# Kernel tuning notes

Hardware: AMD Instinct MI355X
Metric: run time of the kernel (lower is better)

The kernel has to match this reference:

```python
import jax, jax.numpy as jnp
import numpy as np

B, L, D, C, NL = 32, 512, 768, 97, 2  # batch, seq_len, hidden, class_nums, gat_layers


def setup_inputs() -> dict:
    key = jax.random.key(0)
    ks = jax.random.split(key, 16)

    def n(k, shape, scale=0.02):
        return jax.random.normal(k, shape, dtype=jnp.float32) * scale

    return dict(
        x=n(ks[0], (B, L, D), 1.0),                 # encoder output
        pos1=jnp.ones((B, L), jnp.float32),          # entity-1 position mask
        pos2=jnp.ones((B, L), jnp.float32),          # entity-2 position mask
        mask=jnp.ones((B, L), jnp.int32),            # attention mask (1 = keep)
        emb=n(ks[1], (C, D), 1.0),                   # relation label embedding table
        rel_w=n(ks[2], (D, D)), rel_b=jnp.zeros((D,), jnp.float32),
        # per-layer, per-RA (axis1: 0=ra1, 1=ra2) parameters
        qw=n(ks[3], (NL, 2, D, D)), qb=jnp.zeros((NL, 2, D), jnp.float32),
        kw=n(ks[4], (NL, 2, D, D)), kb=jnp.zeros((NL, 2, D), jnp.float32),
        vw=n(ks[5], (NL, 2, D, D)), vb=jnp.zeros((NL, 2, D), jnp.float32),
        sw=n(ks[6], (NL, 2, 2 * D)), sb=jnp.zeros((NL, 2), jnp.float32),   # score: Linear(2d,1)
        gw=n(ks[7], (NL, 2, 2 * D)), gb=jnp.zeros((NL, 2), jnp.float32),   # gate:  Linear(2d,1)
        fc1_w=n(ks[8], (3 * D, D)), fc1_b=jnp.zeros((D,), jnp.float32),
        fc2_w=n(ks[9], (D,)), fc2_b=jnp.zeros((), jnp.float32),
    )


def _relation_attention(p, x, qw, qb, kw, kb, vw, vb, sw, sb, gw, gb, mask):
    # p: (b, c, d) queries; x: (b, l, d) keys/values
    d = p.shape[-1]
    q = jnp.einsum('bcd,de->bce', p, qw) + qb          # (b, c, d)
    k = jnp.einsum('bld,de->ble', x, kw) + kb          # (b, l, d)
    # score = Linear(concat([q_i, k_j])) is separable: q@sw[:d] + k@sw[d:] + sb
    score = (q @ sw[:d])[:, :, None] + (k @ sw[d:])[:, None, :] + sb  # (b, c, l)
    if mask is not None:
        score = jnp.where(mask[:, None, :] == 0, jnp.float32(-1e9), score)
    attn = jax.nn.softmax(score, axis=2)
    v = jnp.einsum('bld,de->ble', x, vw) + vb          # (b, l, d)
    out = jnp.einsum('bcl,bld->bcd', attn, v) + p      # (b, c, d)
    # gate = sigmoid(Linear(concat([out, p]))), also separable
    g = jax.nn.sigmoid(out @ gw[:d] + p @ gw[d:] + gb)[..., None]
    return g * out + (1.0 - g) * p


def reference(x, pos1, pos2, mask, emb, rel_w, rel_b,
              qw, qb, kw, kb, vw, vb, sw, sb, gw, gb,
              fc1_w, fc1_b, fc2_w, fc2_b):
    b, d = x.shape[0], x.shape[-1]
    # p = relation(embedding(arange(C))) broadcast over batch
    p = emb @ rel_w + rel_b                            # (C, d)
    p = jnp.broadcast_to(p[None], (b,) + p.shape)      # (b, C, d)

    for li in range(qw.shape[0]):
        x = _relation_attention(x, p, qw[li, 0], qb[li, 0], kw[li, 0], kb[li, 0],
                                vw[li, 0], vb[li, 0], sw[li, 0], sb[li, 0],
                                gw[li, 0], gb[li, 0], None) + x
        p = _relation_attention(p, x, qw[li, 1], qb[li, 1], kw[li, 1], kb[li, 1],
                                vw[li, 1], vb[li, 1], sw[li, 1], sb[li, 1],
                                gw[li, 1], gb[li, 1], mask) + p

    def pool_avg(pos):
        return jnp.sum(x * pos[:, :, None], axis=1) / jnp.sum(pos, axis=1)[:, None]

    e1 = pool_avg(pos1)                                # (b, d)
    e2 = pool_avg(pos2)                                # (b, d)
    cshape = p.shape                                   # (b, C, d)
    pc = jnp.concatenate([p,
                          jnp.broadcast_to(e1[:, None, :], cshape),
                          jnp.broadcast_to(e2[:, None, :], cshape)], axis=2)  # (b, C, 3d)
    h = jnp.tanh(pc @ fc1_w + fc1_b)                   # (b, C, d)
    logits = jax.nn.sigmoid(h @ fc2_w + fc2_b)         # (b, C)
    pred = jnp.argmax(logits, axis=1)                  # (b,)
    return logits, pred
```

## Files before the change

### kernel.cpp

```cpp
#include <hip/hip_runtime.h>
#include <math.h>

#define NBLK 512
#define NTHR 256
static const int Bb = 32, Ls = 512, Dd = 768, Cc = 97;

struct KArgs {
    const float *x0, *pos1, *pos2;
    const int* mask;
    const float *emb, *rel_w, *rel_b, *kw, *vw, *vb, *sw, *gw, *gb;
    const float *fc1w, *fc1b, *fc2w, *fc2b;
    float* out;
    float *p0b, *pp, *sc, *avx1, *avx2, *av1, *av2, *aw1, *aw2, *S0, *S1, *xp1, *xp2, *geb;
    float *kvecs, *pdots, *g1buf, *xd, *gx1, *gx2, *awb;
    float* zbase;
    int zcount;
};

__device__ __forceinline__ float sigm(float x) { return 1.f / (1.f + expf(-x)); }

__device__ __forceinline__ float wred(float v) {
#pragma unroll
    for (int o = 32; o > 0; o >>= 1) v += __shfl_down(v, o, 64);
    return v;
}

__device__ __forceinline__ float blk_sum4(float v, float* shr) {
    v = wred(v);
    int t = threadIdx.x;
    if ((t & 63) == 0) shr[t >> 6] = v;
    __syncthreads();
    float r = shr[0] + shr[1] + shr[2] + shr[3];
    __syncthreads();
    return r;
}

__device__ void sgemm_dev(const float* __restrict__ A, const float* __restrict__ W,
                          const float* __restrict__ bias, float* __restrict__ C,
                          int M, int N, int K, int KC, int bx, int by, int bz,
                          float* As, float* Ws) {
    int tid = threadIdx.x;
    int tx = tid & 15, ty = tid >> 4;
    int bn = bx * 64, bm = by * 64;
    int kb = bz * KC;
    int arow = tid >> 2, akq = (tid & 3) << 2;
    int wrow = tid >> 4, wcol = (tid & 15) << 2;
    int gar = bm + arow;
    bool aval = gar < M;
    const float* Ap = A + (size_t)gar * K + kb + akq;
    const float* Wp = W + (size_t)(kb + wrow) * N + bn + wcol;
    float acc[4][4] = {{0.f}};
    float4 a4 = make_float4(0.f, 0.f, 0.f, 0.f);
    if (aval) a4 = *(const float4*)Ap;
    float4 w4 = *(const float4*)Wp;
    for (int k0 = 0; k0 < KC; k0 += 16) {
        __syncthreads();
        As[(akq + 0) * 64 + arow] = a4.x; As[(akq + 1) * 64 + arow] = a4.y;
        As[(akq + 2) * 64 + arow] = a4.z; As[(akq + 3) * 64 + arow] = a4.w;
        *(float4*)&Ws[wrow * 64 + wcol] = w4;
        __syncthreads();
        if (k0 + 16 < KC) {
            if (aval) a4 = *(const float4*)(Ap + k0 + 16);
            w4 = *(const float4*)(Wp + (size_t)(k0 + 16) * N);
        }
#pragma unroll
        for (int kk = 0; kk < 16; ++kk) {
            float4 a = *(const float4*)&As[kk * 64 + (ty << 2)];
            float4 b = *(const float4*)&Ws[kk * 64 + (tx << 2)];
            acc[0][0]+=a.x*b.x; acc[0][1]+=a.x*b.y; acc[0][2]+=a.x*b.z; acc[0][3]+=a.x*b.w;
            acc[1][0]+=a.y*b.x; acc[1][1]+=a.y*b.y; acc[1][2]+=a.y*b.z; acc[1][3]+=a.y*b.w;
            acc[2][0]+=a.z*b.x; acc[2][1]+=a.z*b.y; acc[2][2]+=a.z*b.z; acc[2][3]+=a.z*b.w;
            acc[3][0]+=a.w*b.x; acc[3][1]+=a.w*b.y; acc[3][2]+=a.w*b.z; acc[3][3]+=a.w*b.w;
        }
    }
    int gc = bn + (tx << 2);
    float4 bz4 = make_float4(0.f, 0.f, 0.f, 0.f);
    if (bz == 0 && bias) bz4 = *(const float4*)(bias + gc);
#pragma unroll
    for (int i = 0; i < 4; ++i) {
        int gr = bm + (ty << 2) + i;
        if (gr < M) {
            float* cp = C + (size_t)gr * N + gc;
            atomicAdd(cp + 0, acc[i][0] + bz4.x); atomicAdd(cp + 1, acc[i][1] + bz4.y);
            atomicAdd(cp + 2, acc[i][2] + bz4.z); atomicAdd(cp + 3, acc[i][3] + bz4.w);
        }
    }
}

__device__ void attn_gemv(const KArgs& a, int phase, int jlin,
                          float* xs, float* lw, float* shr) {
    int t = threadIdx.x;
    int jseg = jlin % 3, b = (jlin / 3) % 32, seg = jlin / 96;
    float v = -3.0e38f, g1 = 0.f;
    if (t < Cc) {
        if (phase == 0) v = a.pdots[t];
        else {
            g1 = sigm(a.pdots[194 + t] + a.sc[128 + b] + a.gb[1]);
            v = 2.f * a.pdots[97 + t] + g1 * a.sc[160 + b];
        }
    }
    if (phase == 1 && jseg == 0 && seg == 0 && t < Cc) a.g1buf[(size_t)b * Cc + t] = g1;
    float m = v;
#pragma unroll
    for (int o = 32; o > 0; o >>= 1) m = fmaxf(m, __shfl_down(m, o, 64));
    if ((t & 63) == 0) shr[t >> 6] = m;
    __syncthreads();
    m = fmaxf(fmaxf(shr[0], shr[1]), fmaxf(shr[2], shr[3]));
    __syncthreads();
    float e = (t < Cc) ? expf(v - m) : 0.f;
    float s = blk_sum4(e, shr);
    float wc = e / s;
    if (t < Cc) lw[t] = wc;
    float cg1 = blk_sum4(wc * g1, shr);
    float alpha = (phase == 0) ? 1.f : 2.f;
    if (t < 192) {
        int d = seg * 192 + t;
        const float* pc = a.p0b + d;
        float acc2 = 0.f;
        for (int c = 0; c < Cc; ++c) acc2 += lw[c] * pc[(size_t)c * Dd];
        float val = alpha * acc2;
        if (phase == 1) val += cg1 * a.av1[(size_t)b * Dd + d];
        xs[t] = val;
    }
    __syncthreads();
    const float* W = a.vw + (size_t)(phase == 0 ? 0 : 2) * Dd * Dd;
    const float* bias = a.vb + (phase == 0 ? 0 : 2) * Dd;
    float* outp = (phase == 0) ? a.avx1 : a.avx2;
    int j = jseg * 256 + t;
    float acc = (seg == 0) ? bias[j] : 0.f;
    const float* wp = W + (size_t)(seg * 192) * Dd + j;
#pragma unroll 4
    for (int dd = 0; dd < 192; ++dd) acc += xs[dd] * wp[(size_t)dd * Dd];
    atomicAdd(&outp[(size_t)b * Dd + j], acc);
    const float* da[4]; const float* db[4]; int nd; float* dout;
    if (phase == 0) {
        da[0]=a.gw;          db[0]=nullptr;
        da[1]=a.kvecs+Dd;    db[1]=nullptr;
        da[2]=a.gw+3072;     db[2]=a.gw+3840;
        da[3]=a.kvecs+3*Dd;  db[3]=nullptr;
        nd = 4; dout = a.sc;
    } else {
        da[0]=a.gw+3072;     db[0]=nullptr;
        da[1]=a.kvecs+3*Dd;  db[1]=nullptr;
        nd = 2; dout = a.sc + 224;
    }
    for (int vv = 0; vv < nd; ++vv) {
        float wv = da[vv][j] + (db[vv] ? db[vv][j] : 0.f);
        float p = blk_sum4(acc * wv, shr);
        if (t == 0) atomicAdd(&dout[vv * 32 + b], p);
    }
}

__device__ void mm_dev(const KArgs& a, int jlin, const float* S, float gamma,
                       const float* avA, const float* coefA, float multA,
                       const float* avB, const float* coefB, float multB,
                       const float* W, const float* bias, float* outp,
                       int ndots, const float* d0a, const float* d0b,
                       const float* d1a, const float* d2a, const float* d2b,
                       float* dout, float* xs, float* shr) {
    int t = threadIdx.x;
    int jseg = jlin % 3, b = (jlin / 3) % 32, seg = jlin / 96;
    if (t < 192) {
        int d = seg * 192 + t;
        float v = gamma * S[(size_t)b * Dd + d];
        if (avA) v += multA * coefA[b] * avA[(size_t)b * Dd + d];
        if (avB) v += multB * coefB[b] * avB[(size_t)b * Dd + d];
        xs[t] = v;
    }
    __syncthreads();
    int j = jseg * 256 + t;
    float acc = (seg == 0 && bias) ? bias[j] : 0.f;
    const float* wp = W + (size_t)(seg * 192) * Dd + j;
#pragma unroll 4
    for (int dd = 0; dd < 192; ++dd) acc += xs[dd] * wp[(size_t)dd * Dd];
    atomicAdd(&outp[(size_t)b * Dd + j], acc);
    if (ndots > 0) {
        float wv = d0a[j] + (d0b ? d0b[j] : 0.f);
        float p = blk_sum4(acc * wv, shr);
        if (t == 0) atomicAdd(&dout[b], p);
    }
    if (ndots > 1) {
        float p = blk_sum4(acc * d1a[j], shr);
        if (t == 0) atomicAdd(&dout[32 + b], p);
    }
    if (ndots > 2) {
        float wv = d2a[j] + (d2b ? d2b[j] : 0.f);
        float p = blk_sum4(acc * wv, shr);
        if (t == 0) atomicAdd(&dout[64 + b], p);
    }
    __syncthreads();
}

__device__ void ge_dev(const KArgs& a, int jlin, float* xs, float* xs2) {
    __syncthreads();
    int t = threadIdx.x;
    int jseg = jlin % 3, b = (jlin / 3) % 32, seg = jlin / 96;
    if (t < 192) {
        int d = seg * 192 + t;
        float a1 = a.avx1[(size_t)b * Dd + d], a2 = a.avx2[(size_t)b * Dd + d];
        xs[t]  = (4.f * a.xp1[(size_t)b * Dd + d] + 2.f * a.sc[448 + b] * a1 + a.sc[480 + b] * a2) * a.sc[576 + b];
        xs2[t] = (4.f * a.xp2[(size_t)b * Dd + d] + 2.f * a.sc[512 + b] * a1 + a.sc[544 + b] * a2) * a.sc[608 + b];
    }
    __syncthreads();
    int j = jseg * 256 + t;
    float a1 = 0.f, a2 = 0.f;
    const float* w1 = a.fc1w + (size_t)(Dd + seg * 192) * Dd + j;
    const float* w2 = a.fc1w + (size_t)(2 * Dd + seg * 192) * Dd + j;
#pragma unroll 4
    for (int dd = 0; dd < 192; ++dd) {
        a1 += xs[dd] * w1[(size_t)dd * Dd];
        a2 += xs2[dd] * w2[(size_t)dd * Dd];
    }
    float res = a1 + a2 + (seg == 0 ? a.fc1b[j] : 0.f);
    atomicAdd(&a.geb[(size_t)b * Dd + j], res);
}

__device__ void softgate_dev(const KArgs& a, int phase, int b, float* shr) {
    int t = threadIdx.x;
    float ks[2], ga[2] = {0.f, 0.f}, gb2[2] = {0.f, 0.f};
#pragma unroll
    for (int i = 0; i < 2; ++i) {
        int l = t + (i << 8);
        size_t r = (size_t)b * Ls + l;
        float4 x = *(const float4*)(a.xd + r * 4);
        if (phase == 0) {
            float g = sigm(x.x + a.sc[b] + a.gb[0]);
            a.gx1[r] = g;
            ga[i] = g;
            ks[i] = 2.f * x.y + g * a.sc[32 + b];
        } else {
            float gp = a.gx1[r];
            float g = sigm(2.f * x.z + gp * a.sc[64 + b] + a.sc[224 + b] + a.gb[2]);
            a.gx2[r] = g;
            ga[i] = gp; gb2[i] = g;
            ks[i] = 4.f * x.w + 2.f * gp * a.sc[96 + b] + g * a.sc[256 + b];
        }
        if (a.mask[r] == 0) ks[i] = -1e9f;
    }
    float mx = fmaxf(ks[0], ks[1]);
#pragma unroll
    for (int o = 32; o > 0; o >>= 1) mx = fmaxf(mx, __shfl_down(mx, o, 64));
    if ((t & 63) == 0) shr[t >> 6] = mx;
    __syncthreads();
    mx = fmaxf(fmaxf(shr[0], shr[1]), fmaxf(shr[2], shr[3]));
    __syncthreads();
    float e0 = expf(ks[0] - mx), e1 = expf(ks[1] - mx);
    float s = blk_sum4(e0 + e1, shr);
    float inv = 1.f / s;
    float w0 = e0 * inv, w1 = e1 * inv;
    a.awb[(size_t)b * Ls + t] = w0;
    a.awb[(size_t)b * Ls + t + 256] = w1;
    float ca = blk_sum4(w0 * ga[0] + w1 * ga[1], shr);
    if (phase == 0) {
        if (t == 0) a.sc[320 + b] = ca;
    } else {
        if (t == 0) a.sc[352 + b] = ca;
        float cb = blk_sum4(w0 * gb2[0] + w1 * gb2[1], shr);
        if (t == 0) a.sc[384 + b] = cb;
        float q1a = a.pos1[(size_t)b * Ls + t], q1b = a.pos1[(size_t)b * Ls + t + 256];
        float q2a = a.pos2[(size_t)b * Ls + t], q2b = a.pos2[(size_t)b * Ls + t + 256];
        float s1 = blk_sum4(q1a + q1b, shr);
        float s2 = blk_sum4(q2a + q2b, shr);
        float c11 = blk_sum4(q1a * ga[0] + q1b * ga[1], shr);
        float c12 = blk_sum4(q1a * gb2[0] + q1b * gb2[1], shr);
        float c21 = blk_sum4(q2a * ga[0] + q2b * ga[1], shr);
        float c22 = blk_sum4(q2a * gb2[0] + q2b * gb2[1], shr);
        if (t == 0) {
            a.sc[448 + b] = c11; a.sc[480 + b] = c12;
            a.sc[512 + b] = c21; a.sc[544 + b] = c22;
            a.sc[576 + b] = 1.f / s1; a.sc[608 + b] = 1.f / s2;
        }
    }
}

__device__ void passX_dev(const KArgs& a, int blk, float* S, bool dopos) {
    int t = threadIdx.x;
    int b = blk >> 4, seg = blk & 15, l0 = seg * 32;
    const float* xb = a.x0 + ((size_t)b * Ls + l0) * Dd;
    const float* wb = a.awb + (size_t)b * Ls + l0;
    float s0 = 0.f, s1 = 0.f, s2 = 0.f;
    float p10 = 0.f, p11 = 0.f, p12 = 0.f, p20 = 0.f, p21 = 0.f, p22 = 0.f;
    for (int l = 0; l < 32; ++l) {
        float wv = wb[l];
        float x_0 = xb[(size_t)l * Dd + t];
        float x_1 = xb[(size_t)l * Dd + t + 256];
        float x_2 = xb[(size_t)l * Dd + t + 512];
        s0 += wv * x_0; s1 += wv * x_1; s2 += wv * x_2;
        if (dopos) {
            float q1 = a.pos1[(size_t)b * Ls + l0 + l], q2 = a.pos2[(size_t)b * Ls + l0 + l];
            p10 += q1 * x_0; p11 += q1 * x_1; p12 += q1 * x_2;
            p20 += q2 * x_0; p21 += q2 * x_1; p22 += q2 * x_2;
        }
    }
    atomicAdd(&S[(size_t)b * Dd + t], s0);
    atomicAdd(&S[(size_t)b * Dd + t + 256], s1);
    atomicAdd(&S[(size_t)b * Dd + t + 512], s2);
    if (dopos) {
        atomicAdd(&a.xp1[(size_t)b * Dd + t], p10);
        atomicAdd(&a.xp1[(size_t)b * Dd + t + 256], p11);
        atomicAdd(&a.xp1[(size_t)b * Dd + t + 512], p12);
        atomicAdd(&a.xp2[(size_t)b * Dd + t], p20);
        atomicAdd(&a.xp2[(size_t)b * Dd + t + 256], p21);
        atomicAdd(&a.xp2[(size_t)b * Dd + t + 512], p22);
    }
}

__global__ void k_zero_kvec(KArgs a) {
    int blk = blockIdx.x, t = threadIdx.x;
    int wv_ = t >> 6, lane = t & 63;
    for (size_t i = (size_t)blk * NTHR + t; i < (size_t)a.zcount; i += (size_t)NBLK * NTHR)
        a.zbase[i] = 0.f;
    int g = blk * 4 + wv_;
    for (int rep = 0; rep < 2; ++rep) {
        int dot = g + rep * 2048;
        if (dot < 3072) {
            int idx = dot / Dd, d = dot - idx * Dd;
            const float* row = a.kw + ((size_t)idx * Dd + d) * Dd;
            const float* swk = a.sw + (size_t)idx * 2 * Dd + Dd;
            float sA = 0.f;
            for (int j = lane; j < Dd; j += 64) sA += row[j] * swk[j];
            sA = wred(sA);
            if (lane == 0) a.kvecs[dot] = sA;
        }
    }
}

__global__ void k_gemm1(KArgs a) {
    __shared__ float As[1024], Ws[1024];
    int blk = blockIdx.x;
    sgemm_dev(a.emb, a.rel_w, a.rel_b, a.p0b, Cc, Dd, Dd, 96,
              blk % 12, (blk / 12) % 2, blk / 24, As, Ws);
}

__global__ void k_prep2(KArgs a) {
    __shared__ float As[1024], Ws[1024];
    int blk = blockIdx.x, t = threadIdx.x;
    int wv_ = t >> 6, lane = t & 63;
    if (blk < 96) {
        sgemm_dev(a.p0b, a.fc1w, nullptr, a.pp, Cc, Dd, Dd, 192,
                  blk % 12, (blk / 12) % 2, blk / 24, As, Ws);
    } else if (blk < 128) {
        int g2 = (blk - 96) * 4 + wv_;
        for (int k = 0; k < 4; ++k) {
            int j = g2 + k * 128;
            if (k == 3) { if (g2 >= 4) break; j = 384 + g2; }
            if (j >= 388) continue;
            int vv = j / Cc, r = j - vv * Cc;
            const float* va; const float* vb2 = nullptr;
            if (vv == 0) va = a.kvecs;
            else if (vv == 1) va = a.kvecs + 2 * Dd;
            else if (vv == 2) { va = a.gw + 1536; vb2 = a.gw + 2304; }
            else { va = a.gw + 4608; vb2 = a.gw + 5376; }
            const float* row = a.p0b + (size_t)r * Dd;
            float sA = 0.f;
            for (int jj = lane; jj < Dd; jj += 64)
                sA += row[jj] * (va[jj] + (vb2 ? vb2[jj] : 0.f));
            sA = wred(sA);
            if (lane == 0) a.pdots[j] = sA;
        }
    } else {
        float gs0[12], k1r[12], gs2[12], k3r[12];
#pragma unroll
        for (int k = 0; k < 12; ++k) {
            int d = lane + k * 64;
            gs0[k] = a.gw[d] + a.gw[768 + d];
            k1r[k] = a.kvecs[768 + d];
            gs2[k] = a.gw[3072 + d] + a.gw[3840 + d];
            k3r[k] = a.kvecs[2304 + d];
        }
        int gwv = (blk - 128) * 4 + wv_;
        for (int r = gwv; r < Bb * Ls; r += 1536) {
            const float* xr = a.x0 + (size_t)r * Dd;
            float s0 = 0.f, s1 = 0.f, s2 = 0.f, s3 = 0.f;
#pragma unroll
            for (int k = 0; k < 12; ++k) {
                float xv = xr[lane + k * 64];
                s0 += xv * gs0[k]; s1 += xv * k1r[k];
                s2 += xv * gs2[k]; s3 += xv * k3r[k];
            }
            s0 = wred(s0); s1 = wred(s1); s2 = wred(s2); s3 = wred(s3);
            if (lane == 0) {
                float4 o4 = make_float4(s0, s1, s2, s3);
                *(float4*)(a.xd + (size_t)r * 4) = o4;
            }
        }
    }
}

__global__ void k_attn(KArgs a, int phase) {
    __shared__ float xs[192], lw[128], shr[16];
    attn_gemv(a, phase, blockIdx.x, xs, lw, shr);
}

__global__ void k_softgate(KArgs a, int phase) {
    __shared__ float shr[16];
    softgate_dev(a, phase, blockIdx.x, shr);
}

__global__ void k_passX(KArgs a, int which) {
    passX_dev(a, blockIdx.x, which == 0 ? a.S0 : a.S1, which == 0);
}

__global__ void k_mm0(KArgs a) {
    __shared__ float xs[192], shr[16];
    mm_dev(a, blockIdx.x, a.S0, 2.f, a.avx1, a.sc + 320, 1.f, nullptr, nullptr, 0.f,
           a.vw + (size_t)1 * Dd * Dd, a.vb + Dd, a.av1,
           3, a.gw + 1536, nullptr, a.kvecs + 2 * Dd, a.gw + 4608, a.gw + 5376,
           a.sc + 128, xs, shr);
}

__global__ void k_mm1ge(KArgs a) {
    __shared__ float xs[192], xs2[192], shr[16];
    int blk = blockIdx.x;
    if (blk < 384)
        mm_dev(a, blk, a.S1, 4.f, a.avx1, a.sc + 352, 2.f, a.avx2, a.sc + 384, 1.f,
               a.vw + (size_t)3 * Dd * Dd, a.vb + 3 * Dd, a.av2,
               1, a.gw + 4608, nullptr, nullptr, nullptr, nullptr,
               a.sc + 288, xs, shr);
    if (blk >= 128) ge_dev(a, blk - 128, xs, xs2);
}

__global__ void k_aw(KArgs a) {
    __shared__ float xs[192], shr[16];
    int blk = blockIdx.x;
    if (blk < 384)
        mm_dev(a, blk, a.av1, 1.f, nullptr, nullptr, 0.f, nullptr, nullptr, 0.f,
               a.fc1w, nullptr, a.aw1, 0, nullptr, nullptr, nullptr, nullptr, nullptr,
               nullptr, xs, shr);
    else
        mm_dev(a, blk - 384, a.av2, 1.f, nullptr, nullptr, 0.f, nullptr, nullptr, 0.f,
               a.fc1w, nullptr, a.aw2, 0, nullptr, nullptr, nullptr, nullptr, nullptr,
               nullptr, xs, shr);
}

__global__ void k_logits(KArgs a) {
    __shared__ float shr[16];
    int blk = blockIdx.x, t = threadIdx.x;
    for (int r = blk; r < Bb * Cc; r += NBLK) {
        int b = r / Cc, c = r - b * Cc;
        float g1 = a.g1buf[r];
        float g2 = sigm(2.f * a.pdots[291 + c] + g1 * a.sc[192 + b] + a.sc[288 + b] + a.gb[3]);
        float ssum = 0.f;
#pragma unroll
        for (int sseg = 0; sseg < 3; ++sseg) {
            int d = t + sseg * 256;
            float h = tanhf(4.f * a.pp[(size_t)c * Dd + d]
                          + 2.f * g1 * a.aw1[(size_t)b * Dd + d]
                          + g2 * a.aw2[(size_t)b * Dd + d]
                          + a.geb[(size_t)b * Dd + d]);
            ssum += h * a.fc2w[d];
        }
        float tt = blk_sum4(ssum, shr);
        if (t == 0) a.out[r] = sigm(tt + a.fc2b[0]);
    }
}

__global__ void k_argmax(KArgs a) {
    int t = threadIdx.x;
    if (t < Bb) {
        const float* row = a.out + (size_t)t * Cc;
        float best = row[0];
        int bi = 0;
        for (int c = 1; c < Cc; ++c) {
            float v = row[c];
            if (v > best) { best = v; bi = c; }
        }
        a.out[Bb * Cc + t] = (float)bi;
    }
}

extern "C" void kernel_launch(void* const* d_in, const int* in_sizes, int n_in,
                              void* d_out, int out_size, void* d_ws, size_t ws_size,
                              hipStream_t stream) {
    KArgs ka;
    ka.x0    = (const float*)d_in[0];
    ka.pos1  = (const float*)d_in[1];
    ka.pos2  = (const float*)d_in[2];
    ka.mask  = (const int*)d_in[3];
    ka.emb   = (const float*)d_in[4];
    ka.rel_w = (const float*)d_in[5];
    ka.rel_b = (const float*)d_in[6];
    ka.kw    = (const float*)d_in[9];
    ka.vw    = (const float*)d_in[11];
    ka.vb    = (const float*)d_in[12];
    ka.sw    = (const float*)d_in[13];
    ka.gw    = (const float*)d_in[15];
    ka.gb    = (const float*)d_in[16];
    ka.fc1w  = (const float*)d_in[17];
    ka.fc1b  = (const float*)d_in[18];
    ka.fc2w  = (const float*)d_in[19];
    ka.fc2b  = (const float*)d_in[20];
    ka.out   = (float*)d_out;

    float* ws = (float*)d_ws;
    size_t off = 0;
    const size_t PD = (size_t)Cc * Dd;
    const size_t BD = (size_t)Bb * Dd;
    ka.p0b  = ws + off; off += PD;
    ka.pp   = ws + off; off += PD;
    ka.sc   = ws + off; off += 640;
    ka.avx1 = ws + off; off += BD;
    ka.avx2 = ws + off; off += BD;
    ka.av1  = ws + off; off += BD;
    ka.av2  = ws + off; off += BD;
    ka.aw1  = ws + off; off += BD;
    ka.aw2  = ws + off; off += BD;
    ka.S0   = ws + off; off += BD;
    ka.S1   = ws + off; off += BD;
    ka.xp1  = ws + off; off += BD;
    ka.xp2  = ws + off; off += BD;
    ka.geb  = ws + off; off += BD;
    ka.zbase = ws;
    ka.zcount = (int)off;
    ka.kvecs = ws + off; off += (size_t)4 * Dd;
    ka.pdots = ws + off; off += 388;
    ka.g1buf = ws + off; off += (size_t)Bb * Cc;
    ka.xd    = ws + off; off += (size_t)Bb * Ls * 4;
    ka.gx1   = ws + off; off += (size_t)Bb * Ls;
    ka.gx2   = ws + off; off += (size_t)Bb * Ls;
    ka.awb   = ws + off; off += (size_t)Bb * Ls;

    k_zero_kvec<<<NBLK, NTHR, 0, stream>>>(ka);
    k_gemm1<<<192, NTHR, 0, stream>>>(ka);
    k_prep2<<<NBLK, NTHR, 0, stream>>>(ka);
    k_attn<<<384, NTHR, 0, stream>>>(ka, 0);
    k_softgate<<<32, NTHR, 0, stream>>>(ka, 0);
    k_passX<<<NBLK, NTHR, 0, stream>>>(ka, 0);
    k_mm0<<<384, NTHR, 0, stream>>>(ka);
    k_attn<<<384, NTHR, 0, stream>>>(ka, 1);
    k_softgate<<<32, NTHR, 0, stream>>>(ka, 1);
    k_passX<<<NBLK, NTHR, 0, stream>>>(ka, 1);
    k_mm1ge<<<NBLK, NTHR, 0, stream>>>(ka);
    k_aw<<<768, NTHR, 0, stream>>>(ka);
    k_logits<<<NBLK, NTHR, 0, stream>>>(ka);
    k_argmax<<<1, 64, 0, stream>>>(ka);
}
```

Measured before the change: 383.9 us.

## Split GEMV K-range finer, vectorize passX/prep2, fuse aw dual and regroup kernels

The K segment of each GEMV shrinks from 192 to 96, so the attention, mm and ge kernels launch twice as many blocks, which adds parallelism at the cost of more atomic adds. passX and prep2 now use float4 loads. The two aw GEMVs are merged into one kernel that loads each fc1 weight once for both outputs. passX1 is launched together with ge, and mm1 becomes its own kernel, with launch bounds added throughout.

```diff
diff --git a/kernel.cpp b/kernel.cpp
--- a/kernel.cpp
+++ b/kernel.cpp
@@ -90,7 +90,7 @@
 __device__ void attn_gemv(const KArgs& a, int phase, int jlin,
                           float* xs, float* lw, float* shr) {
     int t = threadIdx.x;
-    int jseg = jlin % 3, b = (jlin / 3) % 32, seg = jlin / 96;
+    int jt = jlin % 3, b = (jlin / 3) % 32, kseg = jlin / 96;
     float v = -3.0e38f, g1 = 0.f;
     if (t < Cc) {
         if (phase == 0) v = a.pdots[t];
@@ -99,7 +99,7 @@
             v = 2.f * a.pdots[97 + t] + g1 * a.sc[160 + b];
         }
     }
-    if (phase == 1 && jseg == 0 && seg == 0 && t < Cc) a.g1buf[(size_t)b * Cc + t] = g1;
+    if (phase == 1 && jt == 0 && kseg == 0 && t < Cc) a.g1buf[(size_t)b * Cc + t] = g1;
     float m = v;
 #pragma unroll
     for (int o = 32; o > 0; o >>= 1) m = fmaxf(m, __shfl_down(m, o, 64));
@@ -113,10 +113,11 @@
     if (t < Cc) lw[t] = wc;
     float cg1 = blk_sum4(wc * g1, shr);
     float alpha = (phase == 0) ? 1.f : 2.f;
-    if (t < 192) {
-        int d = seg * 192 + t;
+    if (t < 96) {
+        int d = kseg * 96 + t;
         const float* pc = a.p0b + d;
         float acc2 = 0.f;
+#pragma unroll 4
         for (int c = 0; c < Cc; ++c) acc2 += lw[c] * pc[(size_t)c * Dd];
         float val = alpha * acc2;
         if (phase == 1) val += cg1 * a.av1[(size_t)b * Dd + d];
@@ -126,11 +127,11 @@
     const float* W = a.vw + (size_t)(phase == 0 ? 0 : 2) * Dd * Dd;
     const float* bias = a.vb + (phase == 0 ? 0 : 2) * Dd;
     float* outp = (phase == 0) ? a.avx1 : a.avx2;
-    int j = jseg * 256 + t;
-    float acc = (seg == 0) ? bias[j] : 0.f;
-    const float* wp = W + (size_t)(seg * 192) * Dd + j;
-#pragma unroll 4
-    for (int dd = 0; dd < 192; ++dd) acc += xs[dd] * wp[(size_t)dd * Dd];
+    int j = jt * 256 + t;
+    float acc = (kseg == 0) ? bias[j] : 0.f;
+    const float* wp = W + (size_t)(kseg * 96) * Dd + j;
+#pragma unroll 8
+    for (int dd = 0; dd < 96; ++dd) acc += xs[dd] * wp[(size_t)dd * Dd];
     atomicAdd(&outp[(size_t)b * Dd + j], acc);
     const float* da[4]; const float* db[4]; int nd; float* dout;
     if (phase == 0) {
@@ -159,20 +160,20 @@
                        const float* d1a, const float* d2a, const float* d2b,
                        float* dout, float* xs, float* shr) {
     int t = threadIdx.x;
-    int jseg = jlin % 3, b = (jlin / 3) % 32, seg = jlin / 96;
-    if (t < 192) {
-        int d = seg * 192 + t;
+    int jt = jlin % 3, b = (jlin / 3) % 32, kseg = jlin / 96;
+    if (t < 96) {
+        int d = kseg * 96 + t;
         float v = gamma * S[(size_t)b * Dd + d];
         if (avA) v += multA * coefA[b] * avA[(size_t)b * Dd + d];
         if (avB) v += multB * coefB[b] * avB[(size_t)b * Dd + d];
         xs[t] = v;
     }
     __syncthreads();
-    int j = jseg * 256 + t;
-    float acc = (seg == 0 && bias) ? bias[j] : 0.f;
-    const float* wp = W + (size_t)(seg * 192) * Dd + j;
-#pragma unroll 4
-    for (int dd = 0; dd < 192; ++dd) acc += xs[dd] * wp[(size_t)dd * Dd];
+    int j = jt * 256 + t;
+    float acc = (kseg == 0 && bias) ? bias[j] : 0.f;
+    const float* wp = W + (size_t)(kseg * 96) * Dd + j;
+#pragma unroll 8
+    for (int dd = 0; dd < 96; ++dd) acc += xs[dd] * wp[(size_t)dd * Dd];
     atomicAdd(&outp[(size_t)b * Dd + j], acc);
     if (ndots > 0) {
         float wv = d0a[j] + (d0b ? d0b[j] : 0.f);
@@ -188,31 +189,51 @@
         float p = blk_sum4(acc * wv, shr);
         if (t == 0) atomicAdd(&dout[64 + b], p);
     }
-    __syncthreads();
 }
 
 __device__ void ge_dev(const KArgs& a, int jlin, float* xs, float* xs2) {
-    __syncthreads();
-    int t = threadIdx.x;
-    int jseg = jlin % 3, b = (jlin / 3) % 32, seg = jlin / 96;
-    if (t < 192) {
-        int d = seg * 192 + t;
+    int t = threadIdx.x;
+    int jt = jlin % 3, b = (jlin / 3) % 32, kseg = jlin / 96;
+    if (t < 96) {
+        int d = kseg * 96 + t;
         float a1 = a.avx1[(size_t)b * Dd + d], a2 = a.avx2[(size_t)b * Dd + d];
         xs[t]  = (4.f * a.xp1[(size_t)b * Dd + d] + 2.f * a.sc[448 + b] * a1 + a.sc[480 + b] * a2) * a.sc[576 + b];
         xs2[t] = (4.f * a.xp2[(size_t)b * Dd + d] + 2.f * a.sc[512 + b] * a1 + a.sc[544 + b] * a2) * a.sc[608 + b];
     }
     __syncthreads();
-    int j = jseg * 256 + t;
+    int j = jt * 256 + t;
     float a1 = 0.f, a2 = 0.f;
-    const float* w1 = a.fc1w + (size_t)(Dd + seg * 192) * Dd + j;
-    const float* w2 = a.fc1w + (size_t)(2 * Dd + seg * 192) * Dd + j;
-#pragma unroll 4
-    for (int dd = 0; dd < 192; ++dd) {
+    const float* w1 = a.fc1w + (size_t)(Dd + kseg * 96) * Dd + j;
+    const float* w2 = a.fc1w + (size_t)(2 * Dd + kseg * 96) * Dd + j;
+#pragma unroll 8
+    for (int dd = 0; dd < 96; ++dd) {
         a1 += xs[dd] * w1[(size_t)dd * Dd];
         a2 += xs2[dd] * w2[(size_t)dd * Dd];
     }
-    float res = a1 + a2 + (seg == 0 ? a.fc1b[j] : 0.f);
+    float res = a1 + a2 + (kseg == 0 ? a.fc1b[j] : 0.f);
     atomicAdd(&a.geb[(size_t)b * Dd + j], res);
+}
+
+__device__ void aw_dual_dev(const KArgs& a, int jlin, float* xs, float* xs2) {
+    int t = threadIdx.x;
+    int jt = jlin % 3, b = (jlin / 3) % 32, kseg = jlin / 96;
+    if (t < 96) {
+        int d = kseg * 96 + t;
+        xs[t]  = a.av1[(size_t)b * Dd + d];
+        xs2[t] = a.av2[(size_t)b * Dd + d];
+    }
+    __syncthreads();
+    int j = jt * 256 + t;
+    float a1 = 0.f, a2 = 0.f;
+    const float* wp = a.fc1w + (size_t)(kseg * 96) * Dd + j;
+#pragma unroll 8
+    for (int dd = 0; dd < 96; ++dd) {
+        float w = wp[(size_t)dd * Dd];
+        a1 += xs[dd] * w;
+        a2 += xs2[dd] * w;
+    }
+    atomicAdd(&a.aw1[(size_t)b * Dd + j], a1);
+    atomicAdd(&a.aw2[(size_t)b * Dd + j], a2);
 }
 
 __device__ void softgate_dev(const KArgs& a, int phase, int b, float* shr) {
@@ -275,37 +296,35 @@
 
 __device__ void passX_dev(const KArgs& a, int blk, float* S, bool dopos) {
     int t = threadIdx.x;
+    if (t >= 192) return;
     int b = blk >> 4, seg = blk & 15, l0 = seg * 32;
-    const float* xb = a.x0 + ((size_t)b * Ls + l0) * Dd;
+    int d4 = t << 2;
+    const float* xb = a.x0 + ((size_t)b * Ls + l0) * Dd + d4;
     const float* wb = a.awb + (size_t)b * Ls + l0;
-    float s0 = 0.f, s1 = 0.f, s2 = 0.f;
-    float p10 = 0.f, p11 = 0.f, p12 = 0.f, p20 = 0.f, p21 = 0.f, p22 = 0.f;
+    float4 as = make_float4(0.f,0.f,0.f,0.f);
+    float4 a1 = make_float4(0.f,0.f,0.f,0.f);
+    float4 a2 = make_float4(0.f,0.f,0.f,0.f);
     for (int l = 0; l < 32; ++l) {
+        float4 xv = *(const float4*)(xb + (size_t)l * Dd);
         float wv = wb[l];
-        float x_0 = xb[(size_t)l * Dd + t];
-        float x_1 = xb[(size_t)l * Dd + t + 256];
-        float x_2 = xb[(size_t)l * Dd + t + 512];
-        s0 += wv * x_0; s1 += wv * x_1; s2 += wv * x_2;
+        as.x += wv*xv.x; as.y += wv*xv.y; as.z += wv*xv.z; as.w += wv*xv.w;
         if (dopos) {
             float q1 = a.pos1[(size_t)b * Ls + l0 + l], q2 = a.pos2[(size_t)b * Ls + l0 + l];
-            p10 += q1 * x_0; p11 += q1 * x_1; p12 += q1 * x_2;
-            p20 += q2 * x_0; p21 += q2 * x_1; p22 += q2 * x_2;
-        }
-    }
-    atomicAdd(&S[(size_t)b * Dd + t], s0);
-    atomicAdd(&S[(size_t)b * Dd + t + 256], s1);
-    atomicAdd(&S[(size_t)b * Dd + t + 512], s2);
+            a1.x += q1*xv.x; a1.y += q1*xv.y; a1.z += q1*xv.z; a1.w += q1*xv.w;
+            a2.x += q2*xv.x; a2.y += q2*xv.y; a2.z += q2*xv.z; a2.w += q2*xv.w;
+        }
+    }
+    float* ds = S + (size_t)b * Dd + d4;
+    atomicAdd(ds+0, as.x); atomicAdd(ds+1, as.y); atomicAdd(ds+2, as.z); atomicAdd(ds+3, as.w);
     if (dopos) {
-        atomicAdd(&a.xp1[(size_t)b * Dd + t], p10);
-        atomicAdd(&a.xp1[(size_t)b * Dd + t + 256], p11);
-        atomicAdd(&a.xp1[(size_t)b * Dd + t + 512], p12);
-        atomicAdd(&a.xp2[(size_t)b * Dd + t], p20);
-        atomicAdd(&a.xp2[(size_t)b * Dd + t + 256], p21);
-        atomicAdd(&a.xp2[(size_t)b * Dd + t + 512], p22);
-    }
-}
-
-__global__ void k_zero_kvec(KArgs a) {
+        float* d1 = a.xp1 + (size_t)b * Dd + d4;
+        float* d2 = a.xp2 + (size_t)b * Dd + d4;
+        atomicAdd(d1+0, a1.x); atomicAdd(d1+1, a1.y); atomicAdd(d1+2, a1.z); atomicAdd(d1+3, a1.w);
+        atomicAdd(d2+0, a2.x); atomicAdd(d2+1, a2.y); atomicAdd(d2+2, a2.z); atomicAdd(d2+3, a2.w);
+    }
+}
+
+__global__ __launch_bounds__(NTHR) void k_zero_kvec(KArgs a) {
     int blk = blockIdx.x, t = threadIdx.x;
     int wv_ = t >> 6, lane = t & 63;
     for (size_t i = (size_t)blk * NTHR + t; i < (size_t)a.zcount; i += (size_t)NBLK * NTHR)
@@ -325,14 +344,14 @@
     }
 }
 
-__global__ void k_gemm1(KArgs a) {
+__global__ __launch_bounds__(NTHR) void k_gemm1(KArgs a) {
     __shared__ float As[1024], Ws[1024];
     int blk = blockIdx.x;
     sgemm_dev(a.emb, a.rel_w, a.rel_b, a.p0b, Cc, Dd, Dd, 96,
               blk % 12, (blk / 12) % 2, blk / 24, As, Ws);
 }
 
-__global__ void k_prep2(KArgs a) {
+__global__ __launch_bounds__(NTHR) void k_prep2(KArgs a) {
     __shared__ float As[1024], Ws[1024];
     int blk = blockIdx.x, t = threadIdx.x;
     int wv_ = t >> 6, lane = t & 63;
@@ -359,24 +378,30 @@
             if (lane == 0) a.pdots[j] = sA;
         }
     } else {
-        float gs0[12], k1r[12], gs2[12], k3r[12];
-#pragma unroll
-        for (int k = 0; k < 12; ++k) {
-            int d = lane + k * 64;
-            gs0[k] = a.gw[d] + a.gw[768 + d];
-            k1r[k] = a.kvecs[768 + d];
-            gs2[k] = a.gw[3072 + d] + a.gw[3840 + d];
-            k3r[k] = a.kvecs[2304 + d];
+        float4 gs0[3], k1r[3], gs2[3], k3r[3];
+#pragma unroll
+        for (int k = 0; k < 3; ++k) {
+            int d = (lane << 2) + k * 256;
+            float4 ga = *(const float4*)(a.gw + d);
+            float4 gbv = *(const float4*)(a.gw + 768 + d);
+            gs0[k] = make_float4(ga.x+gbv.x, ga.y+gbv.y, ga.z+gbv.z, ga.w+gbv.w);
+            k1r[k] = *(const float4*)(a.kvecs + 768 + d);
+            float4 g2a = *(const float4*)(a.gw + 3072 + d);
+            float4 g2b = *(const float4*)(a.gw + 3840 + d);
+            gs2[k] = make_float4(g2a.x+g2b.x, g2a.y+g2b.y, g2a.z+g2b.z, g2a.w+g2b.w);
+            k3r[k] = *(const float4*)(a.kvecs + 2304 + d);
         }
         int gwv = (blk - 128) * 4 + wv_;
         for (int r = gwv; r < Bb * Ls; r += 1536) {
             const float* xr = a.x0 + (size_t)r * Dd;
             float s0 = 0.f, s1 = 0.f, s2 = 0.f, s3 = 0.f;
 #pragma unroll
-            for (int k = 0; k < 12; ++k) {
-                float xv = xr[lane + k * 64];
-                s0 += xv * gs0[k]; s1 += xv * k1r[k];
-                s2 += xv * gs2[k]; s3 += xv * k3r[k];
+            for (int k = 0; k < 3; ++k) {
+                float4 xv = *(const float4*)(xr + (lane << 2) + k * 256);
+                s0 += xv.x*gs0[k].x + xv.y*gs0[k].y + xv.z*gs0[k].z + xv.w*gs0[k].w;
+                s1 += xv.x*k1r[k].x + xv.y*k1r[k].y + xv.z*k1r[k].z + xv.w*k1r[k].w;
+                s2 += xv.x*gs2[k].x + xv.y*gs2[k].y + xv.z*gs2[k].z + xv.w*gs2[k].w;
+                s3 += xv.x*k3r[k].x + xv.y*k3r[k].y + xv.z*k3r[k].z + xv.w*k3r[k].w;
             }
             s0 = wred(s0); s1 = wred(s1); s2 = wred(s2); s3 = wred(s3);
             if (lane == 0) {
@@ -387,53 +412,49 @@
     }
 }
 
-__global__ void k_attn(KArgs a, int phase) {
-    __shared__ float xs[192], lw[128], shr[16];
+__global__ __launch_bounds__(NTHR) void k_attn(KArgs a, int phase) {
+    __shared__ float xs[96], lw[128], shr[16];
     attn_gemv(a, phase, blockIdx.x, xs, lw, shr);
 }
 
-__global__ void k_softgate(KArgs a, int phase) {
+__global__ __launch_bounds__(NTHR) void k_softgate(KArgs a, int phase) {
     __shared__ float shr[16];
     softgate_dev(a, phase, blockIdx.x, shr);
 }
 
-__global__ void k_passX(KArgs a, int which) {
-    passX_dev(a, blockIdx.x, which == 0 ? a.S0 : a.S1, which == 0);
-}
-
-__global__ void k_mm0(KArgs a) {
-    __shared__ float xs[192], shr[16];
+__global__ __launch_bounds__(NTHR) void k_passX0(KArgs a) {
+    passX_dev(a, blockIdx.x, a.S0, true);
+}
+
+__global__ __launch_bounds__(NTHR) void k_mm0(KArgs a) {
+    __shared__ float xs[96], shr[16];
     mm_dev(a, blockIdx.x, a.S0, 2.f, a.avx1, a.sc + 320, 1.f, nullptr, nullptr, 0.f,
            a.vw + (size_t)1 * Dd * Dd, a.vb + Dd, a.av1,
            3, a.gw + 1536, nullptr, a.kvecs + 2 * Dd, a.gw + 4608, a.gw + 5376,
            a.sc + 128, xs, shr);
 }
 
-__global__ void k_mm1ge(KArgs a) {
-    __shared__ float xs[192], xs2[192], shr[16];
+__global__ __launch_bounds__(NTHR) void k_passX1ge(KArgs a) {
+    __shared__ float xs[96], xs2[96];
     int blk = blockIdx.x;
-    if (blk < 384)
-        mm_dev(a, blk, a.S1, 4.f, a.avx1, a.sc + 352, 2.f, a.avx2, a.sc + 384, 1.f,
-               a.vw + (size_t)3 * Dd * Dd, a.vb + 3 * Dd, a.av2,
-               1, a.gw + 4608, nullptr, nullptr, nullptr, nullptr,
-               a.sc + 288, xs, shr);
-    if (blk >= 128) ge_dev(a, blk - 128, xs, xs2);
-}
-
-__global__ void k_aw(KArgs a) {
-    __shared__ float xs[192], shr[16];
-    int blk = blockIdx.x;
-    if (blk < 384)
-        mm_dev(a, blk, a.av1, 1.f, nullptr, nullptr, 0.f, nullptr, nullptr, 0.f,
-               a.fc1w, nullptr, a.aw1, 0, nullptr, nullptr, nullptr, nullptr, nullptr,
-               nullptr, xs, shr);
-    else
-        mm_dev(a, blk - 384, a.av2, 1.f, nullptr, nullptr, 0.f, nullptr, nullptr, 0.f,
-               a.fc1w, nullptr, a.aw2, 0, nullptr, nullptr, nullptr, nullptr, nullptr,
-               nullptr, xs, shr);
-}
-
-__global__ void k_logits(KArgs a) {
+    if (blk < 512) passX_dev(a, blk, a.S1, false);
+    else ge_dev(a, blk - 512, xs, xs2);
+}
+
+__global__ __launch_bounds__(NTHR) void k_mm1(KArgs a) {
+    __shared__ float xs[96], shr[16];
+    mm_dev(a, blockIdx.x, a.S1, 4.f, a.avx1, a.sc + 352, 2.f, a.avx2, a.sc + 384, 1.f,
+           a.vw + (size_t)3 * Dd * Dd, a.vb + 3 * Dd, a.av2,
+           1, a.gw + 4608, nullptr, nullptr, nullptr, nullptr,
+           a.sc + 288, xs, shr);
+}
+
+__global__ __launch_bounds__(NTHR) void k_awdual(KArgs a) {
+    __shared__ float xs[96], xs2[96];
+    aw_dual_dev(a, blockIdx.x, xs, xs2);
+}
+
+__global__ __launch_bounds__(NTHR) void k_logits(KArgs a) {
     __shared__ float shr[16];
     int blk = blockIdx.x, t = threadIdx.x;
     for (int r = blk; r < Bb * Cc; r += NBLK) {
@@ -523,15 +544,15 @@
     k_zero_kvec<<<NBLK, NTHR, 0, stream>>>(ka);
     k_gemm1<<<192, NTHR, 0, stream>>>(ka);
     k_prep2<<<NBLK, NTHR, 0, stream>>>(ka);
-    k_attn<<<384, NTHR, 0, stream>>>(ka, 0);
+    k_attn<<<768, NTHR, 0, stream>>>(ka, 0);
     k_softgate<<<32, NTHR, 0, stream>>>(ka, 0);
-    k_passX<<<NBLK, NTHR, 0, stream>>>(ka, 0);
-    k_mm0<<<384, NTHR, 0, stream>>>(ka);
-    k_attn<<<384, NTHR, 0, stream>>>(ka, 1);
+    k_passX0<<<NBLK, NTHR, 0, stream>>>(ka);
+    k_mm0<<<768, NTHR, 0, stream>>>(ka);
+    k_attn<<<768, NTHR, 0, stream>>>(ka, 1);
     k_softgate<<<32, NTHR, 0, stream>>>(ka, 1);
-    k_passX<<<NBLK, NTHR, 0, stream>>>(ka, 1);
-    k_mm1ge<<<NBLK, NTHR, 0, stream>>>(ka);
-    k_aw<<<768, NTHR, 0, stream>>>(ka);
+    k_passX1ge<<<1280, NTHR, 0, stream>>>(ka);
+    k_mm1<<<768, NTHR, 0, stream>>>(ka);
+    k_awdual<<<768, NTHR, 0, stream>>>(ka);
     k_logits<<<NBLK, NTHR, 0, stream>>>(ka);
     k_argmax<<<1, 64, 0, stream>>>(ka);
 }
```

New measurement: 339.4 us. 1.13x faster.
